# Optimization experiments

Measured on AMD Instinct MI355X. Metric: run time of the kernel, lower is better.

Reference implementation:

```python
import jax, jax.numpy as jnp
import numpy as np


def _bilinear_translate(img, tx, ty):
    """Translate a single [H,W] image by (tx, ty) pixels (tfa.image.translate
    convention: out(y, x) = in(y - ty, x - tx)), bilinear sampling, 0 fill."""
    H, W = img.shape
    ys = jnp.arange(H, dtype=img.dtype)[:, None] - ty  # [H,1] source rows
    xs = jnp.arange(W, dtype=img.dtype)[None, :] - tx  # [1,W] source cols
    y0f = jnp.floor(ys)
    x0f = jnp.floor(xs)
    wy = ys - y0f  # [H,1] fractional weights
    wx = xs - x0f  # [1,W]
    y0 = y0f.astype(jnp.int32)
    x0 = x0f.astype(jnp.int32)

    def corner(yi, xi):
        valid = (yi >= 0) & (yi <= H - 1) & (xi >= 0) & (xi <= W - 1)  # [H,W]
        v = img[jnp.clip(yi, 0, H - 1), jnp.clip(xi, 0, W - 1)]       # [H,W]
        return jnp.where(valid, v, jnp.zeros((), img.dtype))

    c00 = corner(y0, x0)
    c01 = corner(y0, x0 + 1)
    c10 = corner(y0 + 1, x0)
    c11 = corner(y0 + 1, x0 + 1)
    return ((1 - wy) * ((1 - wx) * c00 + wx * c01)
            + wy * ((1 - wx) * c10 + wx * c11))


def setup_inputs() -> dict:
    key = jax.random.key(0)
    k1, k2, k3 = jax.random.split(key, 3)
    B, T, H, W = 16, 64, 256, 256
    images = jax.random.normal(k1, (B, T, H, W), dtype=jnp.float32)
    dx = jax.random.normal(k2, (B, T), dtype=jnp.float32)  # subpixel shifts
    dy = jax.random.normal(k3, (B, T), dtype=jnp.float32)
    winsize = 256  # tiled in original call() but unused by translate_image
    return {"images": images, "dx": dx, "dy": dy, "winsize": winsize}


def reference(images, dx, dy, winsize):
    B, T, H, W = images.shape
    flat = images.reshape(B * T, H, W)
    out = jax.vmap(_bilinear_translate)(flat, dx.reshape(-1), dy.reshape(-1))
    return out.reshape(B, T, H, W)
```

## Files before the change

### kernel.cpp

```cpp
#include <hip/hip_runtime.h>


constexpr int HH = 256;
constexpr int WW = 256;
constexpr int RB = 16;
constexpr int SROWS = RB + 1;
constexpr int LW  = 260;
constexpr int LW4 = LW / 4;

__global__ __launch_bounds__(256) void translate_kernel(
    const float* __restrict__ img,
    const float* __restrict__ dx,
    const float* __restrict__ dy,
    float* __restrict__ out)
{
    __shared__ __align__(16) float lds[SROWS][LW];

    const int n  = blockIdx.x >> 4;
    const int yb = (blockIdx.x & 15) * RB;

    const float tx = dx[n];
    const float ty = dy[n];

    const float fxf = floorf(-tx);
    const float fyf = floorf(-ty);
    const float wx  = (-tx) - fxf;
    const float wy  = (-ty) - fyf;
    const float omwx = 1.0f - wx;
    const float omwy = 1.0f - wy;
    const int sx = (int)fxf;
    const int sy = (int)fyf;
    const int astart = sx & ~3;
    const int off    = sx - astart;
    const int rmin   = yb + sy;

    const int tid = threadIdx.x;
    const float* __restrict__ base = img + (size_t)n * (HH * WW);
    for (int idx = tid; idx < SROWS * LW4; idx += 256) {
        const int rr   = idx / LW4;
        const int cc   = idx - rr * LW4;
        const int srow = rmin + rr;
        const int g    = astart + (cc << 2);
        float4 v = make_float4(0.f, 0.f, 0.f, 0.f);
        if ((unsigned)srow < (unsigned)HH) {
            const float* __restrict__ rowp = base + srow * WW;
            if ((unsigned)g <= (unsigned)(WW - 4)) {
                v = *(const float4*)(rowp + g);
            } else {
                const int g0 = g, g1 = g + 1, g2 = g + 2, g3 = g + 3;
                v.x = ((unsigned)g0 < (unsigned)WW) ? rowp[g0] : 0.f;
                v.y = ((unsigned)g1 < (unsigned)WW) ? rowp[g1] : 0.f;
                v.z = ((unsigned)g2 < (unsigned)WW) ? rowp[g2] : 0.f;
                v.w = ((unsigned)g3 < (unsigned)WW) ? rowp[g3] : 0.f;
            }
        }
        *(float4*)&lds[rr][cc << 2] = v;
    }
    __syncthreads();

    const int lane = tid & 63;
    const int wv   = tid >> 6;

    #pragma unroll
    for (int jr = 0; jr < 4; ++jr) {
        const int r = (wv << 2) | jr;
        const int y = yb + r;
        const float* __restrict__ L0 = &lds[r][off];
        const float* __restrict__ L1 = &lds[r + 1][off];
        float* __restrict__ orow = out + ((size_t)n * HH + y) * WW;

        #pragma unroll
        for (int k = 0; k < 4; ++k) {
            const int x = (k << 6) | lane;
            const float c00 = L0[x];
            const float c01 = L0[x + 1];
            const float c10 = L1[x];
            const float c11 = L1[x + 1];
            const float top = omwx * c00 + wx * c01;
            const float bot = omwx * c10 + wx * c11;
            orow[x] = omwy * top + wy * bot;
        }
    }
}

extern "C" void kernel_launch(void* const* d_in, const int* in_sizes, int n_in,
                              void* d_out, int out_size, void* d_ws, size_t ws_size,
                              hipStream_t stream) {
    const float* img = (const float*)d_in[0];
    const float* dx  = (const float*)d_in[1];
    const float* dy  = (const float*)d_in[2];
    float* out = (float*)d_out;

    const int BT = in_sizes[1];
    const int nblocks = BT * (HH / RB);

    translate_kernel<<<nblocks, 256, 0, stream>>>(img, dx, dy, out);
}
```

Before: 434.2 us.

## Replace LDS staging with per-wave register-streamed row bands

```diff
diff --git a/kernel.cpp b/kernel.cpp
--- a/kernel.cpp
+++ b/kernel.cpp
@@ -1,12 +1,89 @@
 #include <hip/hip_runtime.h>
 
 
-constexpr int HH = 256;
-constexpr int WW = 256;
-constexpr int RB = 16;
-constexpr int SROWS = RB + 1;
-constexpr int LW  = 260;
-constexpr int LW4 = LW / 4;
+constexpr int HH  = 256;
+constexpr int WW  = 256;
+constexpr int RPW = 32;
+
+__device__ __forceinline__ void load_row(const float* __restrict__ base, int R,
+                                         int g, int g2, bool gok, bool g2ok,
+                                         float4& V0, float4& V1)
+{
+    V0 = make_float4(0.f, 0.f, 0.f, 0.f);
+    V1 = make_float4(0.f, 0.f, 0.f, 0.f);
+    if ((unsigned)R < (unsigned)HH) {
+        const float* __restrict__ rp = base + R * WW;
+        if (gok)  V0 = *(const float4*)(rp + g);
+        if (g2ok) V1 = *(const float4*)(rp + g2);
+    }
+}
+
+template<int OFF>
+__device__ __forceinline__ float4 xinterp(const float4& V0, const float4& V1,
+                                          float wx, float omwx)
+{
+    float c00x, c00y, c00z, c00w, c01x, c01y, c01z, c01w;
+    if constexpr (OFF == 0) {
+        c00x=V0.x; c00y=V0.y; c00z=V0.z; c00w=V0.w;
+        c01x=V0.y; c01y=V0.z; c01z=V0.w; c01w=V1.x;
+    } else if constexpr (OFF == 1) {
+        c00x=V0.y; c00y=V0.z; c00z=V0.w; c00w=V1.x;
+        c01x=V0.z; c01y=V0.w; c01z=V1.x; c01w=V1.y;
+    } else if constexpr (OFF == 2) {
+        c00x=V0.z; c00y=V0.w; c00z=V1.x; c00w=V1.y;
+        c01x=V0.w; c01y=V1.x; c01z=V1.y; c01w=V1.z;
+    } else {
+        c00x=V0.w; c00y=V1.x; c00z=V1.y; c00w=V1.z;
+        c01x=V1.x; c01y=V1.y; c01z=V1.z; c01w=V1.w;
+    }
+    float4 t;
+    t.x = omwx * c00x + wx * c01x;
+    t.y = omwx * c00y + wx * c01y;
+    t.z = omwx * c00z + wx * c01z;
+    t.w = omwx * c00w + wx * c01w;
+    return t;
+}
+
+template<int OFF>
+__device__ __forceinline__ void wave_band(const float* __restrict__ base,
+                                          float* __restrict__ outb,
+                                          int yb, int sy,
+                                          int g, int g2, bool gok, bool g2ok,
+                                          float wx, float omwx,
+                                          float wy, float omwy, int lane)
+{
+    const int R = yb + sy;
+    float4 A0, A1, B0, B1;
+    load_row(base, R,     g, g2, gok, g2ok, A0, A1);
+    load_row(base, R + 1, g, g2, gok, g2ok, B0, B1);
+    float4 tprev = xinterp<OFF>(A0, A1, wx, omwx);
+
+    float* op = outb + (size_t)yb * WW + (lane << 2);
+
+    #pragma unroll 2
+    for (int r = 0; r < RPW - 1; ++r) {
+        float4 C0, C1;
+        load_row(base, R + 2 + r, g, g2, gok, g2ok, C0, C1);
+        const float4 tcur = xinterp<OFF>(B0, B1, wx, omwx);
+        float4 o;
+        o.x = omwy * tprev.x + wy * tcur.x;
+        o.y = omwy * tprev.y + wy * tcur.y;
+        o.z = omwy * tprev.z + wy * tcur.z;
+        o.w = omwy * tprev.w + wy * tcur.w;
+        *(float4*)op = o;
+        op += WW;
+        tprev = tcur;  B0 = C0;  B1 = C1;
+    }
+    {
+        const float4 tcur = xinterp<OFF>(B0, B1, wx, omwx);
+        float4 o;
+        o.x = omwy * tprev.x + wy * tcur.x;
+        o.y = omwy * tprev.y + wy * tcur.y;
+        o.z = omwy * tprev.z + wy * tcur.z;
+        o.w = omwy * tprev.w + wy * tcur.w;
+        *(float4*)op = o;
+    }
+}
 
 __global__ __launch_bounds__(256) void translate_kernel(
     const float* __restrict__ img,
@@ -14,72 +91,40 @@
     const float* __restrict__ dy,
     float* __restrict__ out)
 {
-    __shared__ __align__(16) float lds[SROWS][LW];
-
-    const int n  = blockIdx.x >> 4;
-    const int yb = (blockIdx.x & 15) * RB;
+    const int n    = blockIdx.x >> 1;
+    const int half = blockIdx.x & 1;
+    const int tid  = threadIdx.x;
+    const int lane = tid & 63;
+    const int wv   = tid >> 6;
+    const int yb   = half * 128 + wv * RPW;
 
     const float tx = dx[n];
     const float ty = dy[n];
 
     const float fxf = floorf(-tx);
     const float fyf = floorf(-ty);
-    const float wx  = (-tx) - fxf;
-    const float wy  = (-ty) - fyf;
+    const float wx   = (-tx) - fxf;
+    const float wy   = (-ty) - fyf;
     const float omwx = 1.0f - wx;
     const float omwy = 1.0f - wy;
     const int sx = (int)fxf;
     const int sy = (int)fyf;
-    const int astart = sx & ~3;
-    const int off    = sx - astart;
-    const int rmin   = yb + sy;
+    const int a   = sx & ~3;
+    const int off = sx - a;
 
-    const int tid = threadIdx.x;
+    const int g  = (lane << 2) + a;
+    const int g2 = g + 4;
+    const bool gok  = (unsigned)g  < (unsigned)WW;
+    const bool g2ok = (unsigned)g2 < (unsigned)WW;
+
     const float* __restrict__ base = img + (size_t)n * (HH * WW);
-    for (int idx = tid; idx < SROWS * LW4; idx += 256) {
-        const int rr   = idx / LW4;
-        const int cc   = idx - rr * LW4;
-        const int srow = rmin + rr;
-        const int g    = astart + (cc << 2);
-        float4 v = make_float4(0.f, 0.f, 0.f, 0.f);
-        if ((unsigned)srow < (unsigned)HH) {
-            const float* __restrict__ rowp = base + srow * WW;
-            if ((unsigned)g <= (unsigned)(WW - 4)) {
-                v = *(const float4*)(rowp + g);
-            } else {
-                const int g0 = g, g1 = g + 1, g2 = g + 2, g3 = g + 3;
-                v.x = ((unsigned)g0 < (unsigned)WW) ? rowp[g0] : 0.f;
-                v.y = ((unsigned)g1 < (unsigned)WW) ? rowp[g1] : 0.f;
-                v.z = ((unsigned)g2 < (unsigned)WW) ? rowp[g2] : 0.f;
-                v.w = ((unsigned)g3 < (unsigned)WW) ? rowp[g3] : 0.f;
-            }
-        }
-        *(float4*)&lds[rr][cc << 2] = v;
-    }
-    __syncthreads();
+    float* __restrict__ outb       = out + (size_t)n * (HH * WW);
 
-    const int lane = tid & 63;
-    const int wv   = tid >> 6;
-
-    #pragma unroll
-    for (int jr = 0; jr < 4; ++jr) {
-        const int r = (wv << 2) | jr;
-        const int y = yb + r;
-        const float* __restrict__ L0 = &lds[r][off];
-        const float* __restrict__ L1 = &lds[r + 1][off];
-        float* __restrict__ orow = out + ((size_t)n * HH + y) * WW;
-
-        #pragma unroll
-        for (int k = 0; k < 4; ++k) {
-            const int x = (k << 6) | lane;
-            const float c00 = L0[x];
-            const float c01 = L0[x + 1];
-            const float c10 = L1[x];
-            const float c11 = L1[x + 1];
-            const float top = omwx * c00 + wx * c01;
-            const float bot = omwx * c10 + wx * c11;
-            orow[x] = omwy * top + wy * bot;
-        }
+    switch (off) {
+        case 0: wave_band<0>(base, outb, yb, sy, g, g2, gok, g2ok, wx, omwx, wy, omwy, lane); break;
+        case 1: wave_band<1>(base, outb, yb, sy, g, g2, gok, g2ok, wx, omwx, wy, omwy, lane); break;
+        case 2: wave_band<2>(base, outb, yb, sy, g, g2, gok, g2ok, wx, omwx, wy, omwy, lane); break;
+        default: wave_band<3>(base, outb, yb, sy, g, g2, gok, g2ok, wx, omwx, wy, omwy, lane); break;
     }
 }
 
@@ -92,7 +137,7 @@
     float* out = (float*)d_out;
 
     const int BT = in_sizes[1];
-    const int nblocks = BT * (HH / RB);
+    const int nblocks = BT * 2;
 
     translate_kernel<<<nblocks, 256, 0, stream>>>(img, dx, dy, out);
 }
```

After: 450.1 us. 3.7% more time.

## Make blocks persistent over eight row bands with register-prefetched loads

Applied to the files above, without the earlier changes.

```diff
diff --git a/kernel.cpp b/kernel.cpp
--- a/kernel.cpp
+++ b/kernel.cpp
@@ -1,5 +1,7 @@
 #include <hip/hip_runtime.h>
 
+
+typedef float f32x4 __attribute__((ext_vector_type(4)));
 
 constexpr int HH = 256;
 constexpr int WW = 256;
@@ -7,6 +9,9 @@
 constexpr int SROWS = RB + 1;
 constexpr int LW  = 260;
 constexpr int LW4 = LW / 4;
+constexpr int NSTG  = SROWS * LW4;
+constexpr int NSLOT = (NSTG + 255) / 256;
+constexpr int BANDS = 8;
 
 __global__ __launch_bounds__(256) void translate_kernel(
     const float* __restrict__ img,
@@ -14,72 +19,101 @@
     const float* __restrict__ dy,
     float* __restrict__ out)
 {
-    __shared__ __align__(16) float lds[SROWS][LW];
+    __shared__ __align__(16) float lds[SROWS * LW + 4];
+    f32x4* const lds4 = (f32x4*)lds;
 
-    const int n  = blockIdx.x >> 4;
-    const int yb = (blockIdx.x & 15) * RB;
+    const int n    = blockIdx.x >> 1;
+    const int half = blockIdx.x & 1;
+    const int tid  = threadIdx.x;
 
     const float tx = dx[n];
     const float ty = dy[n];
-
     const float fxf = floorf(-tx);
     const float fyf = floorf(-ty);
-    const float wx  = (-tx) - fxf;
-    const float wy  = (-ty) - fyf;
+    const float wx   = (-tx) - fxf;
+    const float wy   = (-ty) - fyf;
     const float omwx = 1.0f - wx;
     const float omwy = 1.0f - wy;
     const int sx = (int)fxf;
     const int sy = (int)fyf;
     const int astart = sx & ~3;
     const int off    = sx - astart;
-    const int rmin   = yb + sy;
 
-    const int tid = threadIdx.x;
     const float* __restrict__ base = img + (size_t)n * (HH * WW);
-    for (int idx = tid; idx < SROWS * LW4; idx += 256) {
-        const int rr   = idx / LW4;
-        const int cc   = idx - rr * LW4;
-        const int srow = rmin + rr;
-        const int g    = astart + (cc << 2);
-        float4 v = make_float4(0.f, 0.f, 0.f, 0.f);
-        if ((unsigned)srow < (unsigned)HH) {
-            const float* __restrict__ rowp = base + srow * WW;
-            if ((unsigned)g <= (unsigned)(WW - 4)) {
-                v = *(const float4*)(rowp + g);
-            } else {
-                const int g0 = g, g1 = g + 1, g2 = g + 2, g3 = g + 3;
-                v.x = ((unsigned)g0 < (unsigned)WW) ? rowp[g0] : 0.f;
-                v.y = ((unsigned)g1 < (unsigned)WW) ? rowp[g1] : 0.f;
-                v.z = ((unsigned)g2 < (unsigned)WW) ? rowp[g2] : 0.f;
-                v.w = ((unsigned)g3 < (unsigned)WW) ? rowp[g3] : 0.f;
-            }
-        }
-        *(float4*)&lds[rr][cc << 2] = v;
+    float* __restrict__ outb       = out + (size_t)n * (HH * WW);
+
+    int  s_rr[NSLOT];
+    int  s_adr[NSLOT];
+    int  s_lds[NSLOT];
+    bool s_ok[NSLOT];
+    #pragma unroll
+    for (int s = 0; s < NSLOT; ++s) {
+        const int e = tid + (s << 8);
+        const bool act = (e < NSTG);
+        const int e2 = act ? e : 0;
+        const int rr = e2 / LW4;
+        const int cc = e2 - rr * LW4;
+        const int g  = astart + (cc << 2);
+        s_rr[s]  = rr;
+        s_adr[s] = rr * WW + g;
+        s_lds[s] = act ? e2 : NSTG;
+        s_ok[s]  = act && ((unsigned)g < (unsigned)WW);
     }
-    __syncthreads();
 
     const int lane = tid & 63;
     const int wv   = tid >> 6;
+    const int ybase = half * 128;
 
-    #pragma unroll
-    for (int jr = 0; jr < 4; ++jr) {
-        const int r = (wv << 2) | jr;
-        const int y = yb + r;
-        const float* __restrict__ L0 = &lds[r][off];
-        const float* __restrict__ L1 = &lds[r + 1][off];
-        float* __restrict__ orow = out + ((size_t)n * HH + y) * WW;
+    f32x4 pf[NSLOT];
 
+    auto load_band = [&](int i, f32x4 (&p)[NSLOT]) {
+        const int r0 = ybase + i * RB + sy;
         #pragma unroll
-        for (int k = 0; k < 4; ++k) {
-            const int x = (k << 6) | lane;
-            const float c00 = L0[x];
-            const float c01 = L0[x + 1];
-            const float c10 = L1[x];
-            const float c11 = L1[x + 1];
-            const float top = omwx * c00 + wx * c01;
-            const float bot = omwx * c10 + wx * c11;
-            orow[x] = omwy * top + wy * bot;
+        for (int s = 0; s < NSLOT; ++s) {
+            f32x4 v = {0.f, 0.f, 0.f, 0.f};
+            const int srow = r0 + s_rr[s];
+            if (s_ok[s] && (unsigned)srow < (unsigned)HH)
+                v = *(const f32x4*)(base + r0 * WW + s_adr[s]);
+            p[s] = v;
         }
+    };
+    auto write_band = [&](const f32x4 (&p)[NSLOT]) {
+        #pragma unroll
+        for (int s = 0; s < NSLOT; ++s)
+            lds4[s_lds[s]] = p[s];
+    };
+    auto compute_band = [&](int i) {
+        const int yb = ybase + i * RB;
+        #pragma unroll
+        for (int jr = 0; jr < 4; ++jr) {
+            const int r = (wv << 2) | jr;
+            const float* __restrict__ L0 = &lds[r * LW + off];
+            const float* __restrict__ L1 = L0 + LW;
+            float* __restrict__ orow = outb + (size_t)(yb + r) * WW;
+            #pragma unroll
+            for (int k = 0; k < 4; ++k) {
+                const int x = (k << 6) | lane;
+                const float c00 = L0[x];
+                const float c01 = L0[x + 1];
+                const float c10 = L1[x];
+                const float c11 = L1[x + 1];
+                const float top = omwx * c00 + wx * c01;
+                const float bot = omwx * c10 + wx * c11;
+                __builtin_nontemporal_store(omwy * top + wy * bot, orow + x);
+            }
+        }
+    };
+
+    load_band(0, pf);
+    write_band(pf);
+    __syncthreads();
+
+    for (int i = 0; i < BANDS; ++i) {
+        if (i + 1 < BANDS) load_band(i + 1, pf);
+        compute_band(i);
+        __syncthreads();
+        if (i + 1 < BANDS) write_band(pf);
+        __syncthreads();
     }
 }
 
@@ -92,7 +126,7 @@
     float* out = (float*)d_out;
 
     const int BT = in_sizes[1];
-    const int nblocks = BT * (HH / RB);
+    const int nblocks = BT * 2;
 
     translate_kernel<<<nblocks, 256, 0, stream>>>(img, dx, dy, out);
 }
```

After: 459.8 us. +5.9%, slower.
